# Performance work log

Measured on AMD Instinct MI355X. Metric: run time of the kernel, lower is better.

The kernel has to match this reference:

```python
import jax, jax.numpy as jnp
import numpy as np

# TT-matrix embedding: vocab = 50*60*60 = 180000, embed_dim = 8*8*8 = 512, tt_rank = 16
M1, M2, M3 = 50, 60, 60        # row modes (index factorization)
N1, N2, N3 = 8, 8, 8           # col modes (embedding-dim factorization)
R = 16                         # TT rank
SENT, BATCH = 2048, 64
VOCAB = M1 * M2 * M3


def setup_inputs() -> dict:
    key = jax.random.key(0)
    k1, k2, k3, kx = jax.random.split(key, 4)
    scale = 0.3  # per-core stddev (t3.random_matrix uses a similar per-core normal init)
    # core k stored with the gathered (row-mode) axis first so gather is a plain take
    core1 = jax.random.normal(k1, (M1, N1, R), dtype=jnp.float32) * scale       # [m1, n1, r]
    core2 = jax.random.normal(k2, (M2, R, N2, R), dtype=jnp.float32) * scale    # [m2, r, n2, r]
    core3 = jax.random.normal(k3, (M3, R, N3), dtype=jnp.float32) * scale       # [m3, r, n3]
    x = jax.random.randint(kx, (SENT, BATCH), 0, VOCAB, dtype=jnp.int64)        # batch_dim_last=True layout
    return {"x": x, "core1": core1, "core2": core2, "core3": core3}


def reference(x, core1, core2, core3):
    # batch_dim_last=True: x is [sent, batch] -> permute to [batch, sent]
    sent, batch = x.shape
    flat = x.T.reshape(-1)                      # [T] flat token ids, T = batch*sent
    # t3.ind2sub: row-major mixed-radix decomposition over row modes [M1, M2, M3]
    i1 = flat // (M2 * M3)
    rem = flat % (M2 * M3)
    i2 = rem // M3
    i3 = rem % M3
    # gather one slice per TT core
    g1 = core1[i1]                              # [T, n1, r]
    g2 = core2[i2]                              # [T, r, n2, r]
    g3 = core3[i3]                              # [T, r, n3]
    # contract cores -> full embedding rows (t3.gather_rows(...).full())
    t12 = jnp.einsum('tar,trbs->tabs', g1, g2)  # [T, n1, n2, r]
    emb = jnp.einsum('tabs,tsc->tabc', t12, g3) # [T, n1, n2, n3]
    rows = emb.reshape(batch, sent, N1 * N2 * N3)
    # batch_dim_last=True: permute back to [sent, batch, emb_dim]
    return rows.transpose(1, 0, 2)
```

## Files before the change

kernel.cpp:

```cpp
#include <hip/hip_runtime.h>


#define M2M3  3600u
#define M3    60u
#define NPAIR 3000
#define NPAIR_PAD 3072

__global__ __launch_bounds__(256) void tt_zero(unsigned* __restrict__ counts)
{
    const int i = blockIdx.x * blockDim.x + threadIdx.x;
    if (i < NPAIR_PAD) counts[i] = 0u;
}

__global__ __launch_bounds__(256) void tt_hist(
    const int* __restrict__ x, unsigned* __restrict__ counts, int T)
{
    const int t = blockIdx.x * blockDim.x + threadIdx.x;
    if (t >= T) return;
    const unsigned id = (unsigned)x[t];
    atomicAdd(&counts[id / M3], 1u);
}

__global__ __launch_bounds__(1024) void tt_scan(
    const unsigned* __restrict__ counts, unsigned* __restrict__ cursor)
{
    __shared__ unsigned buf[1024];
    const int tid = threadIdx.x;
    const int b = tid * 3;
    unsigned c0 = 0, c1 = 0, c2 = 0;
    if (b     < NPAIR) c0 = counts[b];
    if (b + 1 < NPAIR) c1 = counts[b + 1];
    if (b + 2 < NPAIR) c2 = counts[b + 2];
    const unsigned local = c0 + c1 + c2;
    buf[tid] = local;
    __syncthreads();
    for (int off = 1; off < 1024; off <<= 1) {
        const unsigned v = (tid >= off) ? buf[tid - off] : 0u;
        __syncthreads();
        buf[tid] += v;
        __syncthreads();
    }
    const unsigned excl = buf[tid] - local;
    if (b     < NPAIR) cursor[b]     = excl;
    if (b + 1 < NPAIR) cursor[b + 1] = excl + c0;
    if (b + 2 < NPAIR) cursor[b + 2] = excl + c0 + c1;
}

__global__ __launch_bounds__(256) void tt_scatter(
    const int* __restrict__ x, unsigned* __restrict__ cursor,
    unsigned* __restrict__ rec, int T)
{
    const int t = blockIdx.x * blockDim.x + threadIdx.x;
    if (t >= T) return;
    const unsigned id   = (unsigned)x[t];
    const unsigned pair = id / M3;
    const unsigned i3   = id - pair * M3;
    const unsigned pos  = atomicAdd(&cursor[pair], 1u);
    rec[pos] = ((unsigned)t << 6) | i3;
}

__global__ __launch_bounds__(256) void tt_embed_grouped(
    const unsigned* __restrict__ rec,
    const unsigned* __restrict__ counts,
    const unsigned* __restrict__ cursor,
    const float* __restrict__ c1,
    const float* __restrict__ c2,
    const float* __restrict__ c3,
    float* __restrict__ out)
{
    const int p    = blockIdx.x;
    const int lane = threadIdx.x & 63;
    const int w    = threadIdx.x >> 6;
    const int a    = lane >> 3;
    const int b    = lane & 7;

    unsigned end = cursor[p];
    unsigned cnt = counts[p];
    end = __builtin_amdgcn_readfirstlane(end);
    cnt = __builtin_amdgcn_readfirstlane(cnt);
    const unsigned start = end - cnt;

    const unsigned q = cnt >> 2, r = cnt & 3u;
    const unsigned nw = q + ((unsigned)w < r ? 1u : 0u);
    if (nw == 0) return;
    const unsigned bw = start + (unsigned)w * q + min((unsigned)w, r);

    const int i1 = p / 60;
    const int i2 = p - i1 * 60;
    const float4* __restrict__ g1v = (const float4*)(c1 + i1 * 128 + a * 16);
    const float*  __restrict__ g2  = c2 + i2 * 2048 + b * 16;

    float4 a1q[4];
#pragma unroll
    for (int k = 0; k < 4; ++k) a1q[k] = g1v[k];
    const float* a1f = (const float*)a1q;

    float4 t4[4];
#pragma unroll
    for (int k = 0; k < 4; ++k) t4[k] = make_float4(0.f, 0.f, 0.f, 0.f);
#pragma unroll
    for (int rr = 0; rr < 16; ++rr) {
        const float a1 = a1f[rr];
        const float4* row = (const float4*)(g2 + rr * 128);
#pragma unroll
        for (int k = 0; k < 4; ++k) {
            const float4 v = row[k];
            t4[k].x = fmaf(a1, v.x, t4[k].x);
            t4[k].y = fmaf(a1, v.y, t4[k].y);
            t4[k].z = fmaf(a1, v.z, t4[k].z);
            t4[k].w = fmaf(a1, v.w, t4[k].w);
        }
    }
    const float* tf = (const float*)t4;

    for (unsigned off = 0; off < nw; off += 64u) {
        const unsigned m = min(64u, nw - off);
        unsigned rj = 0u;
        if ((unsigned)lane < m) rj = rec[bw + off + (unsigned)lane];

        for (unsigned j = 0; j < m; ++j) {
            const unsigned rv = __builtin_amdgcn_readlane(rj, (int)j);
            const unsigned t  = rv >> 6;
            const unsigned i3 = rv & 63u;

            const float4* __restrict__ g3 = (const float4*)(c3 + i3 * 128u);

            float o[8];
#pragma unroll
            for (int c = 0; c < 8; ++c) o[c] = 0.f;
#pragma unroll
            for (int s = 0; s < 16; ++s) {
                const float ts = tf[s];
                const float4 w0 = g3[s * 2 + 0];
                const float4 w1 = g3[s * 2 + 1];
                o[0] = fmaf(ts, w0.x, o[0]);
                o[1] = fmaf(ts, w0.y, o[1]);
                o[2] = fmaf(ts, w0.z, o[2]);
                o[3] = fmaf(ts, w0.w, o[3]);
                o[4] = fmaf(ts, w1.x, o[4]);
                o[5] = fmaf(ts, w1.y, o[5]);
                o[6] = fmaf(ts, w1.z, o[6]);
                o[7] = fmaf(ts, w1.w, o[7]);
            }

            float4* dst = (float4*)(out + (size_t)t * 512u + lane * 8);
            dst[0] = make_float4(o[0], o[1], o[2], o[3]);
            dst[1] = make_float4(o[4], o[5], o[6], o[7]);
        }
    }
}

__global__ __launch_bounds__(256) void tt_pair_kernel(
    const float* __restrict__ c1, const float* __restrict__ c2,
    float* __restrict__ tab)
{
    const int pair = blockIdx.x;
    const int i1 = pair / 60;
    const int i2 = pair - i1 * 60;
    const int tid = threadIdx.x;
    const int qq = tid >> 6;
    const int ab = tid & 63;
    const int a  = ab >> 3;
    const int b  = ab & 7;
    const float* __restrict__ g1 = c1 + i1 * 128 + a * 16;
    const float* __restrict__ g2 = c2 + i2 * 2048 + b * 16 + qq * 4;
    float4 acc = make_float4(0.f, 0.f, 0.f, 0.f);
#pragma unroll
    for (int rr = 0; rr < 16; ++rr) {
        const float a1 = g1[rr];
        const float4 v = *(const float4*)(g2 + rr * 128);
        acc.x = fmaf(a1, v.x, acc.x);
        acc.y = fmaf(a1, v.y, acc.y);
        acc.z = fmaf(a1, v.z, acc.z);
        acc.w = fmaf(a1, v.w, acc.w);
    }
    *(float4*)(tab + (size_t)pair * 1024 + tid * 4) = acc;
}

__global__ __launch_bounds__(256) void tt_embed2_kernel(
    const int* __restrict__ x, const float* __restrict__ c3,
    const float* __restrict__ tab, float* __restrict__ out, int T)
{
    const int u    = (int)((blockIdx.x * blockDim.x + threadIdx.x) >> 6);
    const int lane = threadIdx.x & 63;
    if (u >= T) return;
    const unsigned id  = __builtin_amdgcn_readfirstlane((unsigned)x[u]);
    const unsigned i1  = id / M2M3;
    const unsigned rem = id - i1 * M2M3;
    const unsigned i2  = rem / M3;
    const unsigned i3  = rem - i2 * M3;
    const float* tp = tab + (size_t)(i1 * 60u + i2) * 1024u;
    float4 t[4];
#pragma unroll
    for (int k = 0; k < 4; ++k)
        t[k] = *(const float4*)(tp + k * 256 + lane * 4);
    const float* tf = (const float*)t;
    const float4* __restrict__ g3 = (const float4*)(c3 + i3 * 128u);
    float o[8];
#pragma unroll
    for (int c = 0; c < 8; ++c) o[c] = 0.f;
#pragma unroll
    for (int s = 0; s < 16; ++s) {
        const float ts = tf[s];
        const float4 w0 = g3[s * 2 + 0];
        const float4 w1 = g3[s * 2 + 1];
        o[0]=fmaf(ts,w0.x,o[0]); o[1]=fmaf(ts,w0.y,o[1]);
        o[2]=fmaf(ts,w0.z,o[2]); o[3]=fmaf(ts,w0.w,o[3]);
        o[4]=fmaf(ts,w1.x,o[4]); o[5]=fmaf(ts,w1.y,o[5]);
        o[6]=fmaf(ts,w1.z,o[6]); o[7]=fmaf(ts,w1.w,o[7]);
    }
    float4* dst = (float4*)(out + (size_t)u * 512 + lane * 8);
    dst[0] = make_float4(o[0], o[1], o[2], o[3]);
    dst[1] = make_float4(o[4], o[5], o[6], o[7]);
}

__global__ __launch_bounds__(256) void tt_embed_kernel(
    const int* __restrict__ x, const float* __restrict__ c1,
    const float* __restrict__ c2, const float* __restrict__ c3,
    float* __restrict__ out, int T)
{
    const int u    = (int)((blockIdx.x * blockDim.x + threadIdx.x) >> 6);
    const int lane = threadIdx.x & 63;
    if (u >= T) return;
    const int a = lane >> 3, b = lane & 7;
    const unsigned id  = (unsigned)x[u];
    const unsigned i1  = id / M2M3;
    const unsigned rem = id - i1 * M2M3;
    const unsigned i2  = rem / M3;
    const unsigned i3  = rem - i2 * M3;
    const float4* g1 = (const float4*)(c1 + i1 * 128u + a * 16);
    const float*  g2 = c2 + i2 * 2048u + b * 16;
    const float4* g3 = (const float4*)(c3 + i3 * 128u);
    float4 a1v[4];
#pragma unroll
    for (int k = 0; k < 4; ++k) a1v[k] = g1[k];
    const float* a1f = (const float*)a1v;
    float t12[16];
#pragma unroll
    for (int s = 0; s < 16; ++s) t12[s] = 0.f;
#pragma unroll
    for (int rr = 0; rr < 16; ++rr) {
        const float a1 = a1f[rr];
        const float4* row = (const float4*)(g2 + rr * 128);
#pragma unroll
        for (int k = 0; k < 4; ++k) {
            const float4 v = row[k];
            t12[k*4+0] = fmaf(a1, v.x, t12[k*4+0]);
            t12[k*4+1] = fmaf(a1, v.y, t12[k*4+1]);
            t12[k*4+2] = fmaf(a1, v.z, t12[k*4+2]);
            t12[k*4+3] = fmaf(a1, v.w, t12[k*4+3]);
        }
    }
    float o[8];
#pragma unroll
    for (int c = 0; c < 8; ++c) o[c] = 0.f;
#pragma unroll
    for (int s = 0; s < 16; ++s) {
        const float ts = t12[s];
        const float4 w0 = g3[s*2+0];
        const float4 w1 = g3[s*2+1];
        o[0]=fmaf(ts,w0.x,o[0]); o[1]=fmaf(ts,w0.y,o[1]);
        o[2]=fmaf(ts,w0.z,o[2]); o[3]=fmaf(ts,w0.w,o[3]);
        o[4]=fmaf(ts,w1.x,o[4]); o[5]=fmaf(ts,w1.y,o[5]);
        o[6]=fmaf(ts,w1.z,o[6]); o[7]=fmaf(ts,w1.w,o[7]);
    }
    float4* dst = (float4*)(out + (size_t)u * 512 + lane * 8);
    dst[0] = make_float4(o[0], o[1], o[2], o[3]);
    dst[1] = make_float4(o[4], o[5], o[6], o[7]);
}

extern "C" void kernel_launch(void* const* d_in, const int* in_sizes, int n_in,
                              void* d_out, int out_size, void* d_ws, size_t ws_size,
                              hipStream_t stream) {
    const int*   x  = (const int*)d_in[0];
    const float* c1 = (const float*)d_in[1];
    const float* c2 = (const float*)d_in[2];
    const float* c3 = (const float*)d_in[3];
    float* out = (float*)d_out;

    const int T = in_sizes[0];

    const size_t off_counts = 0;
    const size_t off_cursor = off_counts + (size_t)NPAIR_PAD * 4u;
    const size_t off_rec    = off_cursor + (size_t)NPAIR_PAD * 4u;
    const size_t need_sort  = off_rec + (size_t)T * 4u;
    const size_t tab_bytes  = (size_t)NPAIR * 1024u * sizeof(float);

    char* ws = (char*)d_ws;

    if (ws_size >= need_sort) {
        unsigned* counts = (unsigned*)(ws + off_counts);
        unsigned* cursor = (unsigned*)(ws + off_cursor);
        unsigned* rec    = (unsigned*)(ws + off_rec);

        tt_zero<<<(NPAIR_PAD + 255) / 256, 256, 0, stream>>>(counts);
        tt_hist<<<(T + 255) / 256, 256, 0, stream>>>(x, counts, T);
        tt_scan<<<1, 1024, 0, stream>>>(counts, cursor);
        tt_scatter<<<(T + 255) / 256, 256, 0, stream>>>(x, cursor, rec, T);
        tt_embed_grouped<<<NPAIR, 256, 0, stream>>>(rec, counts, cursor,
                                                    c1, c2, c3, out);
    } else if (ws_size >= tab_bytes) {
        float* tab = (float*)ws;
        tt_pair_kernel<<<NPAIR, 256, 0, stream>>>(c1, c2, tab);
        const int blocks = (T + 3) / 4;
        tt_embed2_kernel<<<blocks, 256, 0, stream>>>(x, c3, tab, out, T);
    } else {
        const int blocks = (T + 3) / 4;
        tt_embed_kernel<<<blocks, 256, 0, stream>>>(x, c1, c2, c3, out, T);
    }
}
```

Before: 324.2 us.

## Fuse counting-sort stages into one cooperative kernel and use nontemporal output stores

The four sort kernels (zero, histogram, scan, scatter) are merged into a single cooperative launch of 256 blocks that separates the phases with grid-wide syncs. This removes three kernel launches and their gaps. The scan now runs in one 256-thread block with 12 elements per thread. The embed kernel also writes its output with nontemporal stores to avoid polluting the cache with the large output, and the original multi-kernel path is kept as a fallback if the cooperative launch fails.

```diff
diff --git a/kernel.cpp b/kernel.cpp
--- a/kernel.cpp
+++ b/kernel.cpp
@@ -1,4 +1,7 @@
 #include <hip/hip_runtime.h>
+#include <hip/hip_cooperative_groups.h>
+
+namespace cg = cooperative_groups;
 
 
 #define M2M3  3600u
@@ -6,6 +9,156 @@
 #define NPAIR 3000
 #define NPAIR_PAD 3072
 
+typedef float vf4 __attribute__((ext_vector_type(4)));
+
+__global__ __launch_bounds__(256) void tt_sort_coop(
+    const int* __restrict__ x,
+    unsigned* __restrict__ counts,
+    unsigned* __restrict__ cursor,
+    unsigned* __restrict__ rec,
+    int T)
+{
+    cg::grid_group grid = cg::this_grid();
+    const int tid = blockIdx.x * blockDim.x + threadIdx.x;
+    const int nth = gridDim.x * blockDim.x;
+
+    for (int i = tid; i < NPAIR_PAD; i += nth) counts[i] = 0u;
+    grid.sync();
+
+    for (int t = tid; t < T; t += nth)
+        atomicAdd(&counts[(unsigned)x[t] / M3], 1u);
+    grid.sync();
+
+    if (blockIdx.x == 0) {
+        __shared__ unsigned part[256];
+        const int base = threadIdx.x * 12;
+        unsigned v[12];
+        unsigned s = 0;
+#pragma unroll
+        for (int k = 0; k < 12; ++k) {
+            const unsigned c = (base + k < NPAIR) ? counts[base + k] : 0u;
+            v[k] = s;
+            s += c;
+        }
+        part[threadIdx.x] = s;
+        __syncthreads();
+        unsigned inc = s;
+        for (int off = 1; off < 256; off <<= 1) {
+            const unsigned add = (threadIdx.x >= off) ? part[threadIdx.x - off] : 0u;
+            __syncthreads();
+            inc += add;
+            part[threadIdx.x] = inc;
+            __syncthreads();
+        }
+        const unsigned chunk_excl = inc - s;
+#pragma unroll
+        for (int k = 0; k < 12; ++k)
+            if (base + k < NPAIR) cursor[base + k] = chunk_excl + v[k];
+    }
+    grid.sync();
+
+    for (int t = tid; t < T; t += nth) {
+        const unsigned id   = (unsigned)x[t];
+        const unsigned pair = id / M3;
+        const unsigned i3   = id - pair * M3;
+        const unsigned pos  = atomicAdd(&cursor[pair], 1u);
+        rec[pos] = ((unsigned)t << 6) | i3;
+    }
+}
+
+__global__ __launch_bounds__(256) void tt_embed_grouped(
+    const unsigned* __restrict__ rec,
+    const unsigned* __restrict__ counts,
+    const unsigned* __restrict__ cursor,
+    const float* __restrict__ c1,
+    const float* __restrict__ c2,
+    const float* __restrict__ c3,
+    float* __restrict__ out)
+{
+    const int p    = blockIdx.x;
+    const int lane = threadIdx.x & 63;
+    const int w    = threadIdx.x >> 6;
+    const int a    = lane >> 3;
+    const int b    = lane & 7;
+
+    unsigned end = cursor[p];
+    unsigned cnt = counts[p];
+    end = __builtin_amdgcn_readfirstlane(end);
+    cnt = __builtin_amdgcn_readfirstlane(cnt);
+    const unsigned start = end - cnt;
+
+    const unsigned q = cnt >> 2, r = cnt & 3u;
+    const unsigned nw = q + ((unsigned)w < r ? 1u : 0u);
+    if (nw == 0) return;
+    const unsigned bw = start + (unsigned)w * q + min((unsigned)w, r);
+
+    const int i1 = p / 60;
+    const int i2 = p - i1 * 60;
+    const float4* __restrict__ g1v = (const float4*)(c1 + i1 * 128 + a * 16);
+    const float*  __restrict__ g2  = c2 + i2 * 2048 + b * 16;
+
+    float4 a1q[4];
+#pragma unroll
+    for (int k = 0; k < 4; ++k) a1q[k] = g1v[k];
+    const float* a1f = (const float*)a1q;
+
+    float4 t4[4];
+#pragma unroll
+    for (int k = 0; k < 4; ++k) t4[k] = make_float4(0.f, 0.f, 0.f, 0.f);
+#pragma unroll
+    for (int rr = 0; rr < 16; ++rr) {
+        const float a1 = a1f[rr];
+        const float4* row = (const float4*)(g2 + rr * 128);
+#pragma unroll
+        for (int k = 0; k < 4; ++k) {
+            const float4 v = row[k];
+            t4[k].x = fmaf(a1, v.x, t4[k].x);
+            t4[k].y = fmaf(a1, v.y, t4[k].y);
+            t4[k].z = fmaf(a1, v.z, t4[k].z);
+            t4[k].w = fmaf(a1, v.w, t4[k].w);
+        }
+    }
+    const float* tf = (const float*)t4;
+
+    for (unsigned off = 0; off < nw; off += 64u) {
+        const unsigned m = min(64u, nw - off);
+        unsigned rj = 0u;
+        if ((unsigned)lane < m) rj = rec[bw + off + (unsigned)lane];
+
+        for (unsigned j = 0; j < m; ++j) {
+            const unsigned rv = __builtin_amdgcn_readlane(rj, (int)j);
+            const unsigned t  = rv >> 6;
+            const unsigned i3 = rv & 63u;
+
+            const float4* __restrict__ g3 = (const float4*)(c3 + i3 * 128u);
+
+            float o[8];
+#pragma unroll
+            for (int c = 0; c < 8; ++c) o[c] = 0.f;
+#pragma unroll
+            for (int s = 0; s < 16; ++s) {
+                const float ts = tf[s];
+                const float4 w0 = g3[s * 2 + 0];
+                const float4 w1 = g3[s * 2 + 1];
+                o[0] = fmaf(ts, w0.x, o[0]);
+                o[1] = fmaf(ts, w0.y, o[1]);
+                o[2] = fmaf(ts, w0.z, o[2]);
+                o[3] = fmaf(ts, w0.w, o[3]);
+                o[4] = fmaf(ts, w1.x, o[4]);
+                o[5] = fmaf(ts, w1.y, o[5]);
+                o[6] = fmaf(ts, w1.z, o[6]);
+                o[7] = fmaf(ts, w1.w, o[7]);
+            }
+
+            vf4* dst = (vf4*)(out + (size_t)t * 512u + lane * 8);
+            const vf4 r0 = {o[0], o[1], o[2], o[3]};
+            const vf4 r1 = {o[4], o[5], o[6], o[7]};
+            __builtin_nontemporal_store(r0, dst);
+            __builtin_nontemporal_store(r1, dst + 1);
+        }
+    }
+}
+
 __global__ __launch_bounds__(256) void tt_zero(unsigned* __restrict__ counts)
 {
     const int i = blockIdx.x * blockDim.x + threadIdx.x;
@@ -17,8 +170,7 @@
 {
     const int t = blockIdx.x * blockDim.x + threadIdx.x;
     if (t >= T) return;
-    const unsigned id = (unsigned)x[t];
-    atomicAdd(&counts[id / M3], 1u);
+    atomicAdd(&counts[(unsigned)x[t] / M3], 1u);
 }
 
 __global__ __launch_bounds__(1024) void tt_scan(
@@ -59,97 +211,6 @@
     rec[pos] = ((unsigned)t << 6) | i3;
 }
 
-__global__ __launch_bounds__(256) void tt_embed_grouped(
-    const unsigned* __restrict__ rec,
-    const unsigned* __restrict__ counts,
-    const unsigned* __restrict__ cursor,
-    const float* __restrict__ c1,
-    const float* __restrict__ c2,
-    const float* __restrict__ c3,
-    float* __restrict__ out)
-{
-    const int p    = blockIdx.x;
-    const int lane = threadIdx.x & 63;
-    const int w    = threadIdx.x >> 6;
-    const int a    = lane >> 3;
-    const int b    = lane & 7;
-
-    unsigned end = cursor[p];
-    unsigned cnt = counts[p];
-    end = __builtin_amdgcn_readfirstlane(end);
-    cnt = __builtin_amdgcn_readfirstlane(cnt);
-    const unsigned start = end - cnt;
-
-    const unsigned q = cnt >> 2, r = cnt & 3u;
-    const unsigned nw = q + ((unsigned)w < r ? 1u : 0u);
-    if (nw == 0) return;
-    const unsigned bw = start + (unsigned)w * q + min((unsigned)w, r);
-
-    const int i1 = p / 60;
-    const int i2 = p - i1 * 60;
-    const float4* __restrict__ g1v = (const float4*)(c1 + i1 * 128 + a * 16);
-    const float*  __restrict__ g2  = c2 + i2 * 2048 + b * 16;
-
-    float4 a1q[4];
-#pragma unroll
-    for (int k = 0; k < 4; ++k) a1q[k] = g1v[k];
-    const float* a1f = (const float*)a1q;
-
-    float4 t4[4];
-#pragma unroll
-    for (int k = 0; k < 4; ++k) t4[k] = make_float4(0.f, 0.f, 0.f, 0.f);
-#pragma unroll
-    for (int rr = 0; rr < 16; ++rr) {
-        const float a1 = a1f[rr];
-        const float4* row = (const float4*)(g2 + rr * 128);
-#pragma unroll
-        for (int k = 0; k < 4; ++k) {
-            const float4 v = row[k];
-            t4[k].x = fmaf(a1, v.x, t4[k].x);
-            t4[k].y = fmaf(a1, v.y, t4[k].y);
-            t4[k].z = fmaf(a1, v.z, t4[k].z);
-            t4[k].w = fmaf(a1, v.w, t4[k].w);
-        }
-    }
-    const float* tf = (const float*)t4;
-
-    for (unsigned off = 0; off < nw; off += 64u) {
-        const unsigned m = min(64u, nw - off);
-        unsigned rj = 0u;
-        if ((unsigned)lane < m) rj = rec[bw + off + (unsigned)lane];
-
-        for (unsigned j = 0; j < m; ++j) {
-            const unsigned rv = __builtin_amdgcn_readlane(rj, (int)j);
-            const unsigned t  = rv >> 6;
-            const unsigned i3 = rv & 63u;
-
-            const float4* __restrict__ g3 = (const float4*)(c3 + i3 * 128u);
-
-            float o[8];
-#pragma unroll
-            for (int c = 0; c < 8; ++c) o[c] = 0.f;
-#pragma unroll
-            for (int s = 0; s < 16; ++s) {
-                const float ts = tf[s];
-                const float4 w0 = g3[s * 2 + 0];
-                const float4 w1 = g3[s * 2 + 1];
-                o[0] = fmaf(ts, w0.x, o[0]);
-                o[1] = fmaf(ts, w0.y, o[1]);
-                o[2] = fmaf(ts, w0.z, o[2]);
-                o[3] = fmaf(ts, w0.w, o[3]);
-                o[4] = fmaf(ts, w1.x, o[4]);
-                o[5] = fmaf(ts, w1.y, o[5]);
-                o[6] = fmaf(ts, w1.z, o[6]);
-                o[7] = fmaf(ts, w1.w, o[7]);
-            }
-
-            float4* dst = (float4*)(out + (size_t)t * 512u + lane * 8);
-            dst[0] = make_float4(o[0], o[1], o[2], o[3]);
-            dst[1] = make_float4(o[4], o[5], o[6], o[7]);
-        }
-    }
-}
-
 __global__ __launch_bounds__(256) void tt_pair_kernel(
     const float* __restrict__ c1, const float* __restrict__ c2,
     float* __restrict__ tab)
@@ -293,10 +354,16 @@
         unsigned* cursor = (unsigned*)(ws + off_cursor);
         unsigned* rec    = (unsigned*)(ws + off_rec);
 
-        tt_zero<<<(NPAIR_PAD + 255) / 256, 256, 0, stream>>>(counts);
-        tt_hist<<<(T + 255) / 256, 256, 0, stream>>>(x, counts, T);
-        tt_scan<<<1, 1024, 0, stream>>>(counts, cursor);
-        tt_scatter<<<(T + 255) / 256, 256, 0, stream>>>(x, cursor, rec, T);
+        void* args[] = { (void*)&x, (void*)&counts, (void*)&cursor,
+                         (void*)&rec, (void*)&T };
+        const hipError_t ce = hipLaunchCooperativeKernel(
+            (const void*)tt_sort_coop, dim3(256), dim3(256), args, 0, stream);
+        if (ce != hipSuccess) {
+            tt_zero<<<(NPAIR_PAD + 255) / 256, 256, 0, stream>>>(counts);
+            tt_hist<<<(T + 255) / 256, 256, 0, stream>>>(x, counts, T);
+            tt_scan<<<1, 1024, 0, stream>>>(counts, cursor);
+            tt_scatter<<<(T + 255) / 256, 256, 0, stream>>>(x, cursor, rec, T);
+        }
         tt_embed_grouped<<<NPAIR, 256, 0, stream>>>(rec, counts, cursor,
                                                     c1, c2, c3, out);
     } else if (ws_size >= tab_bytes) {
```

Result: slower. 448.3 us (+38.3%).
